# Optimization experiments

Measured on AMD Instinct MI355X. Metric: run time of the kernel, lower is better.

Reference implementation:

```python
import jax, jax.numpy as jnp
import numpy as np
from jax import lax

C = 512   # n_feat == Cn == Cdim (forced by DA_conv/CA_layer consistency)
H, W = 16, 32  # reshape_codebooks(512)
K = 3     # kernel_size
RED = 8   # reduction


def _lrelu(x):
    return jax.nn.leaky_relu(x, 0.1)


def _conv1x1(x, w, b=None):
    # x: (B,C,H,W), w: (O,C) -- torch Conv2d(.,.,1) weight squeezed
    y = jnp.einsum('oc,bchw->bohw', w, x)
    if b is not None:
        y = y + b[None, :, None, None]
    return y


def _conv3x3(x, w, b):
    # x: (B,C,H,W), w: (O,C,3,3) OIHW, padding=k//2 == SAME for odd k
    y = lax.conv_general_dilated(x, w, (1, 1), 'SAME',
                                 dimension_numbers=('NCHW', 'OIHW', 'NCHW'))
    return y + b[None, :, None, None]


def _da_conv(c, deg, kw1, kw2, pw, pb, caw1, caw2):
    # per-channel dynamic kernels from degradation vectors: (Cn, K*K)
    kern = (_lrelu(deg @ kw1.T) @ kw2.T).reshape(C, 1, K, K)
    # depthwise conv, groups = b1*c1 = C (b1 == 1)
    out = lax.conv_general_dilated(c, kern, (1, 1), 'SAME',
                                   feature_group_count=C,
                                   dimension_numbers=('NCHW', 'OIHW', 'NCHW'))
    out = _lrelu(out)
    out = _conv1x1(out, pw, pb)
    # CA_layer: deg reshaped to (1, Cn, 16, 32), channel attention, deg * att
    dr = deg.reshape(1, C, H, W)
    att = jax.nn.sigmoid(_conv1x1(_lrelu(_conv1x1(dr, caw1)), caw2))
    return out + dr * att


def setup_inputs() -> dict:
    key = jax.random.key(0)
    ks = jax.random.split(key, 16)
    n = lambda i, shape, s=0.05: jax.random.normal(ks[i], shape, dtype=jnp.float32) * s
    return dict(
        c=jax.random.normal(ks[0], (1, C, H, W), dtype=jnp.float32),
        deg=jax.random.normal(ks[1], (C, C), dtype=jnp.float32) * 0.1,
        k1_w1=n(2, (C, C)), k1_w2=n(3, (K * K, C)),
        p1_w=n(4, (C, C)), p1_b=jnp.zeros((C,), jnp.float32),
        ca1_w1=n(5, (C // RED, C)), ca1_w2=n(6, (C, C // RED)),
        conv1_w=n(7, (C, C, K, K)), conv1_b=jnp.zeros((C,), jnp.float32),
        k2_w1=n(8, (C, C)), k2_w2=n(9, (K * K, C)),
        p2_w=n(10, (C, C)), p2_b=jnp.zeros((C,), jnp.float32),
        ca2_w1=n(11, (C // RED, C)), ca2_w2=n(12, (C, C // RED)),
        conv2_w=n(13, (C, C, K, K)), conv2_b=jnp.zeros((C,), jnp.float32),
    )


def reference(c, deg, k1_w1, k1_w2, p1_w, p1_b, ca1_w1, ca1_w2,
              conv1_w, conv1_b, k2_w1, k2_w2, p2_w, p2_b,
              ca2_w1, ca2_w2, conv2_w, conv2_b):
    out = _lrelu(_da_conv(c, deg, k1_w1, k1_w2, p1_w, p1_b, ca1_w1, ca1_w2))
    out = _lrelu(_conv3x3(out, conv1_w, conv1_b))
    out = _lrelu(_da_conv(out, deg, k2_w1, k2_w2, p2_w, p2_b, ca2_w1, ca2_w2))
    return _conv3x3(out, conv2_w, conv2_b) + c
```

## Files before the change

kernel.cpp:

```cpp
#include <hip/hip_runtime.h>
#include <hip/hip_bf16.h>

typedef __attribute__((ext_vector_type(8))) unsigned short ushort8;
typedef __attribute__((ext_vector_type(8))) __bf16 bf16x8;
typedef __attribute__((ext_vector_type(4))) float f32x4;
typedef __attribute__((ext_vector_type(4))) unsigned short ushort4v;

__device__ __forceinline__ float lrelu_f(float v){ return v > 0.f ? v : 0.1f*v; }

__device__ __forceinline__ unsigned short f2bf(float v){
  unsigned u = __float_as_uint(v);
  unsigned r = (u + 0x7fffu + ((u>>16)&1u)) >> 16;
  return (unsigned short)r;
}
__device__ __forceinline__ float bf2f(unsigned short u){
  return __uint_as_float(((unsigned)u)<<16);
}

__device__ __forceinline__ void gload16(const void* g, void* l){
  __builtin_amdgcn_global_load_lds(
    (const __attribute__((address_space(1))) unsigned int*)g,
    (__attribute__((address_space(3))) unsigned int*)l, 16, 0, 0);
}

__device__ __forceinline__ void packq(const float* __restrict__ s,
                                      unsigned short* __restrict__ d, int i){
  const float4 v = ((const float4*)s)[i];
  ushort4v o; o.x=f2bf(v.x); o.y=f2bf(v.y); o.z=f2bf(v.z); o.w=f2bf(v.w);
  *(ushort4v*)(d + (size_t)i*4) = o;
}

__global__ __launch_bounds__(256) void k_pack_all(
  const float* __restrict__ k1_w1, const float* __restrict__ k2_w1,
  const float* __restrict__ p1_w,  const float* __restrict__ p2_w,
  const float* __restrict__ ca1_w1,const float* __restrict__ ca1_w2,
  const float* __restrict__ ca2_w1,const float* __restrict__ ca2_w2,
  const float* __restrict__ deg,   const float* __restrict__ conv1_w,
  const float* __restrict__ conv2_w,
  unsigned short* __restrict__ K1B, unsigned short* __restrict__ K2B,
  unsigned short* __restrict__ P1B, unsigned short* __restrict__ P2B,
  unsigned short* __restrict__ CA1A,unsigned short* __restrict__ CA1B,
  unsigned short* __restrict__ CA2A,unsigned short* __restrict__ CA2B,
  unsigned short* __restrict__ DEGB,unsigned short* __restrict__ DEGT,
  unsigned short* __restrict__ WB1, unsigned short* __restrict__ WB2){
  int i = blockIdx.x*256 + threadIdx.x;
  if (i < 65536){ packq(k1_w1, K1B, i); return; } i -= 65536;
  if (i < 65536){ packq(k2_w1, K2B, i); return; } i -= 65536;
  if (i < 65536){ packq(p1_w,  P1B, i); return; } i -= 65536;
  if (i < 65536){ packq(p2_w,  P2B, i); return; } i -= 65536;
  if (i < 8192){ packq(ca1_w1, CA1A, i); return; } i -= 8192;
  if (i < 8192){ packq(ca1_w2, CA1B, i); return; } i -= 8192;
  if (i < 8192){ packq(ca2_w1, CA2A, i); return; } i -= 8192;
  if (i < 8192){ packq(ca2_w2, CA2B, i); return; } i -= 8192;
  if (i < 65536){ packq(deg, DEGB, i); return; } i -= 65536;
  if (i < 65536){
    const int j = i*4; const int p = j>>9, c = j&511;
    ushort4v o;
    o.x = f2bf(deg[(size_t)(c+0)*512 + p]);
    o.y = f2bf(deg[(size_t)(c+1)*512 + p]);
    o.z = f2bf(deg[(size_t)(c+2)*512 + p]);
    o.w = f2bf(deg[(size_t)(c+3)*512 + p]);
    *(ushort4v*)(DEGT + (size_t)j) = o;
    return;
  } i -= 65536;
  if (i < 589824){
    const int o_ = i/1152; const int r4 = (i - o_*1152)*4;
    const int t = r4>>9; const int ci = r4&511;
    const float* s = conv1_w + (size_t)o_*4608;
    ushort4v o;
    o.x = f2bf(s[(ci+0)*9 + t]); o.y = f2bf(s[(ci+1)*9 + t]);
    o.z = f2bf(s[(ci+2)*9 + t]); o.w = f2bf(s[(ci+3)*9 + t]);
    *(ushort4v*)(WB1 + (size_t)o_*4608 + r4) = o;
    return;
  } i -= 589824;
  if (i < 589824){
    const int o_ = i/1152; const int r4 = (i - o_*1152)*4;
    const int t = r4>>9; const int ci = r4&511;
    const float* s = conv2_w + (size_t)o_*4608;
    ushort4v o;
    o.x = f2bf(s[(ci+0)*9 + t]); o.y = f2bf(s[(ci+1)*9 + t]);
    o.z = f2bf(s[(ci+2)*9 + t]); o.w = f2bf(s[(ci+3)*9 + t]);
    *(ushort4v*)(WB2 + (size_t)o_*4608 + r4) = o;
  }
}

__device__ __forceinline__ void gemm32(
    const unsigned short* __restrict__ A, const unsigned short* __restrict__ Bt,
    int m0, int n0, int K, int tid,
    unsigned short* lA, unsigned short* lB, f32x4& acc){
  const int wid = tid>>6, lane = tid&63;
  const int half = tid>>7, st_ = tid&127;
  const int srow = st_>>2, skb = st_&3;
  const unsigned short* gS = (half ? Bt + (size_t)(n0+srow)*K
                                   : A  + (size_t)(m0+srow)*K);
  unsigned short* lS = half ? lB : lA;
  const int soff0 = srow*64 + 8*(skb ^ (srow&7));
  const int soff1 = srow*64 + 8*((skb+4) ^ (srow&7));

  const int wr = (wid>>1)*16, wc = (wid&1)*16;
  const int l15 = lane&15, lkb = lane>>4;
  int aoff[2], boff[2];
  #pragma unroll
  for (int h=0;h<2;h++){
    const int Ra = wr + l15;
    aoff[h] = Ra*64 + 8*((lkb+4*h) ^ (Ra&7));
    const int Rb = wc + l15;
    boff[h] = Rb*64 + 8*((lkb+4*h) ^ (Rb&7));
  }

  const int nst = K>>6;
  ushort8 r0 = *(const ushort8*)(gS + skb*8);
  ushort8 r1 = *(const ushort8*)(gS + (skb+4)*8);
  *(ushort8*)(lS + soff0) = r0;
  *(ushort8*)(lS + soff1) = r1;
  if (nst > 1){
    r0 = *(const ushort8*)(gS + 64 + skb*8);
    r1 = *(const ushort8*)(gS + 64 + (skb+4)*8);
  }
  __syncthreads();
  for (int st=0; st<nst; ++st){
    const int cur = (st&1)*2048;
    bf16x8 af[2], bf[2];
    #pragma unroll
    for (int h=0;h<2;h++){
      af[h] = *(const bf16x8*)(lA + cur + aoff[h]);
      bf[h] = *(const bf16x8*)(lB + cur + boff[h]);
    }
    if (st+1 < nst){
      const int nxt = ((st+1)&1)*2048;
      *(ushort8*)(lS + nxt + soff0) = r0;
      *(ushort8*)(lS + nxt + soff1) = r1;
      if (st+2 < nst){
        r0 = *(const ushort8*)(gS + (size_t)(st+2)*64 + skb*8);
        r1 = *(const ushort8*)(gS + (size_t)(st+2)*64 + (skb+4)*8);
      }
    }
    #pragma unroll
    for (int h=0;h<2;h++)
      acc = __builtin_amdgcn_mfma_f32_16x16x32_bf16(af[h], bf[h], acc, 0,0,0);
    __syncthreads();
  }
}

__global__ __launch_bounds__(256) void k_mgemm_pre(
    const unsigned short* __restrict__ DEGB, const unsigned short* __restrict__ DEGT,
    const unsigned short* __restrict__ K1B,  const unsigned short* __restrict__ K2B,
    const unsigned short* __restrict__ CA1A, const unsigned short* __restrict__ CA2A,
    float* __restrict__ TMP1, float* __restrict__ TMP2,
    unsigned short* __restrict__ HID1, unsigned short* __restrict__ HID2){
  const int z = blockIdx.z;
  if (z >= 2 && blockIdx.y >= 2) return;
  const unsigned short* A  = (z < 2) ? DEGB : DEGT;
  const unsigned short* Bt = (z==0) ? K1B : (z==1) ? K2B : (z==2) ? CA1A : CA2A;
  __shared__ unsigned short lA[4096], lB[4096];
  const int tid = threadIdx.x;
  const int m0 = blockIdx.x*32, n0 = blockIdx.y*32;
  f32x4 acc = {};
  gemm32(A, Bt, m0, n0, 512, tid, lA, lB, acc);

  const int wid = tid>>6, lane = tid&63;
  const int wr = (wid>>1)*16, wc = (wid&1)*16;
  const int l15 = lane&15, lkb = lane>>4;
  #pragma unroll
  for (int r=0;r<4;r++){
    const int row = m0 + wr + lkb*4 + r;
    const int col = n0 + wc + l15;
    const float v = lrelu_f(acc[r]);
    if (z==0)      TMP1[(size_t)row*512 + col] = v;
    else if (z==1) TMP2[(size_t)row*512 + col] = v;
    else if (z==2) HID1[(size_t)row*64 + col] = f2bf(v);
    else           HID2[(size_t)row*64 + col] = f2bf(v);
  }
}

__device__ __forceinline__ void gemm64(
    const unsigned short* __restrict__ A, const unsigned short* __restrict__ Bt,
    int m0, int n0, int K, int tid,
    unsigned short* lA, unsigned short* lB, f32x4 acc[2][2]){
  const int wid = tid>>6, lane = tid&63;
  const int srow = tid>>2, skb = tid&3;
  const unsigned short* gA = A  + (size_t)(m0+srow)*K + skb*8;
  const unsigned short* gB = Bt + (size_t)(n0+srow)*K + skb*8;
  const int soff = srow*32 + 8*(skb ^ (srow&3));
  const int wr = (wid>>1)*32, wc = (wid&1)*32;
  const int l15 = lane&15, lkb = lane>>4;
  int aoff[2], boff[2];
  #pragma unroll
  for (int s=0;s<2;s++){
    const int Ra = wr + s*16 + l15;
    aoff[s] = Ra*32 + 8*(lkb ^ (Ra&3));
    const int Rb = wc + s*16 + l15;
    boff[s] = Rb*32 + 8*(lkb ^ (Rb&3));
  }
  const int nst = K>>5;
  ushort8 ra = *(const ushort8*)gA;
  ushort8 rb = *(const ushort8*)gB;
  *(ushort8*)(lA + soff) = ra;
  *(ushort8*)(lB + soff) = rb;
  if (nst > 1){ ra = *(const ushort8*)(gA+32); rb = *(const ushort8*)(gB+32); }
  __syncthreads();
  for (int st=0; st<nst; ++st){
    const int cur = (st&1)*2048;
    bf16x8 af[2], bfr[2];
    #pragma unroll
    for (int s=0;s<2;s++){
      af[s]  = *(const bf16x8*)(lA + cur + aoff[s]);
      bfr[s] = *(const bf16x8*)(lB + cur + boff[s]);
    }
    if (st+1 < nst){
      const int nxt = ((st+1)&1)*2048;
      *(ushort8*)(lA + nxt + soff) = ra;
      *(ushort8*)(lB + nxt + soff) = rb;
      if (st+2 < nst){
        ra = *(const ushort8*)(gA + (size_t)(st+2)*32);
        rb = *(const ushort8*)(gB + (size_t)(st+2)*32);
      }
    }
    #pragma unroll
    for (int mi=0;mi<2;mi++)
      #pragma unroll
      for (int ni=0;ni<2;ni++)
        acc[mi][ni] = __builtin_amdgcn_mfma_f32_16x16x32_bf16(af[mi], bfr[ni], acc[mi][ni], 0,0,0);
    __syncthreads();
  }
}

__global__ __launch_bounds__(256) void k_kern_att(
    const float* __restrict__ TMP1, const float* __restrict__ TMP2,
    const float* __restrict__ kw2a, const float* __restrict__ kw2b,
    const unsigned short* __restrict__ CA1B, const unsigned short* __restrict__ CA2B,
    const unsigned short* __restrict__ HID1, const unsigned short* __restrict__ HID2,
    float* __restrict__ kern0, float* __restrict__ kern1,
    float* __restrict__ ATT1, float* __restrict__ ATT2){
  const int z = blockIdx.z;
  const int tid = threadIdx.x;
  if (z < 2){
    const float* tmp  = z ? TMP2 : TMP1;
    const float* kw2  = z ? kw2b : kw2a;
    float* kern       = z ? kern1 : kern0;
    const int i = blockIdx.x*4 + (tid>>6);
    const int lane = tid&63;
    float acc[9];
    #pragma unroll
    for (int q=0;q<9;q++) acc[q]=0.f;
    for (int j=lane; j<512; j+=64){
      const float t = tmp[i*512 + j];
      #pragma unroll
      for (int q=0;q<9;q++) acc[q] += t*kw2[q*512 + j];
    }
    #pragma unroll
    for (int q=0;q<9;q++){
      float v = acc[q];
      #pragma unroll
      for (int off=32; off>0; off>>=1) v += __shfl_down(v, off);
      if (lane==0) kern[i*9+q] = v;
    }
  } else {
    if (blockIdx.x >= 64) return;
    const unsigned short* A  = (z==2) ? CA1B : CA2B;
    const unsigned short* Bt = (z==2) ? HID1 : HID2;
    float* ATT               = (z==2) ? ATT1 : ATT2;
    __shared__ unsigned short lA[4096], lB[4096];
    const int m0 = (blockIdx.x>>3)*64, n0 = (blockIdx.x&7)*64;
    f32x4 acc[2][2] = {};
    gemm64(A, Bt, m0, n0, 64, tid, lA, lB, acc);
    const int wid = tid>>6, lane = tid&63;
    const int wr = (wid>>1)*32, wc = (wid&1)*32;
    const int l15 = lane&15, lkb = lane>>4;
    #pragma unroll
    for (int mi=0;mi<2;mi++)
      #pragma unroll
      for (int ni=0;ni<2;ni++){
        const int row = m0 + wr + mi*16 + lkb*4;
        const int col = n0 + wc + ni*16 + l15;
        #pragma unroll
        for (int r=0;r<4;r++)
          ATT[(size_t)(row+r)*512 + col] = 1.f/(1.f + expf(-acc[mi][ni][r]));
      }
  }
}

__global__ __launch_bounds__(512) void k_dwconv(const float* __restrict__ x,
    const float* __restrict__ kern, unsigned short* __restrict__ yt,
    unsigned short* __restrict__ XTP){
  const int c = blockIdx.x;
  const int p = threadIdx.x;
  const int iy = p>>5, ix = p&31;
  {
    const int idx = blockIdx.x*512 + p;
    if (idx < 12800){
      const int si = idx>>7, wi = idx&127;
      int slot;
      if (si < 34) slot = si;
      else if (si < 68) slot = 578 + (si-34);
      else if (si < 84) slot = (si-67)*34;
      else slot = (si-83)*34 + 33;
      ushort4v z = {};
      *(ushort4v*)(XTP + (size_t)slot*512 + wi*4) = z;
    }
  }
  __shared__ float plane[18*34];
  for (int i=p;i<18*34;i+=512) plane[i]=0.f;
  __syncthreads();
  plane[(iy+1)*34 + ix+1] = x[c*512 + p];
  __syncthreads();
  const float* kp = kern + c*9;
  float s = 0.f;
  #pragma unroll
  for (int dy=0;dy<3;dy++)
    #pragma unroll
    for (int dx=0;dx<3;dx++)
      s += plane[(iy+dy)*34 + ix+dx]*kp[dy*3+dx];
  yt[(size_t)p*512 + c] = f2bf(lrelu_f(s));
}

__global__ __launch_bounds__(512) void k_dwconv_red(const unsigned short* __restrict__ part,
    const float* __restrict__ bias, const float* __restrict__ kern,
    unsigned short* __restrict__ yt, int nchunks){
  const int c = blockIdx.x;
  const int p = threadIdx.x;
  const int iy = p>>5, ix = p&31;
  __shared__ float plane[18*34];
  for (int i=p;i<18*34;i+=512) plane[i]=0.f;
  __syncthreads();
  if (p < 128){
    const float b = bias[c];
    float4 a4 = {b,b,b,b};
    for (int s=0;s<nchunks;s++){
      const ushort4v v = ((const ushort4v*)(part + (size_t)s*262144 + c*512))[p];
      a4.x += bf2f(v.x); a4.y += bf2f(v.y); a4.z += bf2f(v.z); a4.w += bf2f(v.w);
    }
    a4.x = lrelu_f(a4.x); a4.y = lrelu_f(a4.y);
    a4.z = lrelu_f(a4.z); a4.w = lrelu_f(a4.w);
    const int px0 = p*4;
    float* dst = &plane[((px0>>5)+1)*34 + (px0&31)+1];
    dst[0]=a4.x; dst[1]=a4.y; dst[2]=a4.z; dst[3]=a4.w;
  }
  __syncthreads();
  const float* kp = kern + c*9;
  float s = 0.f;
  #pragma unroll
  for (int dy=0;dy<3;dy++)
    #pragma unroll
    for (int dx=0;dx<3;dx++)
      s += plane[(iy+dy)*34 + ix+dx]*kp[dy*3+dx];
  yt[(size_t)p*512 + c] = f2bf(lrelu_f(s));
}

__global__ __launch_bounds__(256) void k_pw(
    const unsigned short* __restrict__ A, const unsigned short* __restrict__ Bt,
    const float* __restrict__ bias,
    const float* __restrict__ E1, const float* __restrict__ E2,
    unsigned short* __restrict__ XTP){
  __shared__ unsigned short lA[4096], lB[4096];
  __shared__ float tile[32][33];
  const int tid = threadIdx.x;
  const int wid = tid>>6, lane = tid&63;
  const int M0 = blockIdx.x*32, N0 = blockIdx.y*32;

  f32x4 acc = {};
  gemm32(A, Bt, M0, N0, 512, tid, lA, lB, acc);

  const int wr = (wid>>1)*16, wc = (wid&1)*16;
  const int l15 = lane&15, lkb = lane>>4;
  #pragma unroll
  for (int r=0;r<4;r++){
    const int rl = wr + lkb*4 + r;
    const int cl = wc + l15;
    const int rr = M0 + rl, col = N0 + cl;
    float v = acc[r] + bias[rr] + E1[(size_t)rr*512+col]*E2[(size_t)rr*512+col];
    tile[rl][cl] = lrelu_f(v);
  }
  __syncthreads();
  const int pr = tid>>3, q = tid&7;
  const int p = N0 + pr;
  const int slot = ((p>>5)+1)*34 + (p&31) + 1;
  ushort4v o;
  o.x = f2bf(tile[q*4+0][pr]); o.y = f2bf(tile[q*4+1][pr]);
  o.z = f2bf(tile[q*4+2][pr]); o.w = f2bf(tile[q*4+3][pr]);
  *(ushort4v*)(XTP + (size_t)slot*512 + M0 + q*4) = o;
}

template<int KCH>
__global__ __launch_bounds__(256) void k_mfma_conv(
    const unsigned short* __restrict__ WB,
    const unsigned short* __restrict__ XTP,
    unsigned short* __restrict__ part){
  __shared__ __attribute__((aligned(16))) unsigned short lA[2][4096];
  __shared__ __attribute__((aligned(16))) unsigned short lB[2][8192];
  const int tid = threadIdx.x;
  const int wid = tid>>6, lane = tid&63;
  const int m0 = blockIdx.x*64, n0 = blockIdx.y*128;
  const int k0 = blockIdx.z*KCH;

  const int wrow = wid*8 + (lane>>3);
  const int clin = lane&7;
  const unsigned short* asrc[2];
  #pragma unroll
  for (int j=0;j<2;j++){
    const int r = j*32 + wrow;
    asrc[j] = WB + (size_t)(m0+r)*4608 + k0 + (clin ^ (r&7))*8;
  }
  int bpy[4], bpx[4], bchk[4];
  #pragma unroll
  for (int j=0;j<4;j++){
    const int r = j*32 + wrow;
    const int pp = n0 + r;
    bpy[j] = pp>>5; bpx[j] = pp&31;
    bchk[j] = (clin ^ (r&7))*8;
  }

  const int wr = (wid>>1)*32, wc = (wid&1)*64;
  const int l15 = lane&15, lkb = lane>>4;
  int aoff[2][2], boff[4][2];
  #pragma unroll
  for (int s=0;s<2;s++){
    const int Ra = wr + s*16 + l15;
    #pragma unroll
    for (int h=0;h<2;h++) aoff[s][h] = Ra*64 + 8*((lkb+4*h) ^ (Ra&7));
  }
  #pragma unroll
  for (int u=0;u<4;u++){
    const int Rb = wc + u*16 + l15;
    #pragma unroll
    for (int h=0;h<2;h++) boff[u][h] = Rb*64 + 8*((lkb+4*h) ^ (Rb&7));
  }

  auto stage = [&](int buf, int st){
    #pragma unroll
    for (int j=0;j<2;j++)
      gload16(asrc[j] + st*64, &lA[buf][j*2048 + wid*512]);
    const int k = k0 + st*64;
    const int t = k>>9;
    const int dy = t/3, dx = t - dy*3;
    const int kc = k & 511;
    #pragma unroll
    for (int j=0;j<4;j++){
      const int slot = (bpy[j]+dy)*34 + bpx[j]+dx;
      gload16(XTP + (size_t)slot*512 + kc + bchk[j],
              &lB[buf][j*2048 + wid*512]);
    }
  };

  constexpr int NST = KCH/64;
  f32x4 acc[2][4] = {};
  stage(0, 0);
  __syncthreads();
  #pragma unroll
  for (int st=0; st<NST; ++st){
    const int cur = st&1;
    if (st+1 < NST) stage(cur^1, st+1);
    bf16x8 af[2][2], bfr[4][2];
    #pragma unroll
    for (int s=0;s<2;s++)
      #pragma unroll
      for (int h=0;h<2;h++) af[s][h] = *(const bf16x8*)(&lA[cur][aoff[s][h]]);
    #pragma unroll
    for (int u=0;u<4;u++)
      #pragma unroll
      for (int h=0;h<2;h++) bfr[u][h] = *(const bf16x8*)(&lB[cur][boff[u][h]]);
    #pragma unroll
    for (int h=0;h<2;h++)
      #pragma unroll
      for (int s=0;s<2;s++)
        #pragma unroll
        for (int u=0;u<4;u++)
          acc[s][u] = __builtin_amdgcn_mfma_f32_16x16x32_bf16(af[s][h], bfr[u][h], acc[s][u], 0,0,0);
    __syncthreads();
  }

  unsigned short* pbase = part + (size_t)blockIdx.z*262144;
  #pragma unroll
  for (int s=0;s<2;s++)
    #pragma unroll
    for (int u=0;u<4;u++){
      const int row = m0 + wr + s*16 + lkb*4;
      const int col = n0 + wc + u*16 + l15;
      #pragma unroll
      for (int r=0;r<4;r++)
        pbase[(size_t)(row+r)*512 + col] = f2bf(acc[s][u][r]);
    }
}

__global__ __launch_bounds__(256) void k_reduce_final(const unsigned short* __restrict__ part,
    const float* __restrict__ bias, const float* __restrict__ res,
    float* __restrict__ y, int nchunks){
  const int i = blockIdx.x*256 + threadIdx.x;
  const int o = i>>7;
  const float b = bias[o];
  float4 a4 = {b,b,b,b};
  for (int s=0;s<nchunks;s++){
    const ushort4v v = ((const ushort4v*)part)[(size_t)s*65536 + i];
    a4.x += bf2f(v.x); a4.y += bf2f(v.y); a4.z += bf2f(v.z); a4.w += bf2f(v.w);
  }
  const float4 rv = ((const float4*)res)[i];
  a4.x += rv.x; a4.y += rv.y; a4.z += rv.z; a4.w += rv.w;
  ((float4*)y)[i] = a4;
}

extern "C" void kernel_launch(void* const* d_in, const int* in_sizes, int n_in,
                              void* d_out, int out_size, void* d_ws, size_t ws_size,
                              hipStream_t stream) {
  (void)in_sizes; (void)n_in; (void)out_size; (void)ws_size;
  const float* xin    = (const float*)d_in[0];
  const float* deg    = (const float*)d_in[1];
  const float* k1_w1  = (const float*)d_in[2];
  const float* k1_w2  = (const float*)d_in[3];
  const float* p1_w   = (const float*)d_in[4];
  const float* p1_b   = (const float*)d_in[5];
  const float* ca1_w1 = (const float*)d_in[6];
  const float* ca1_w2 = (const float*)d_in[7];
  const float* conv1_w= (const float*)d_in[8];
  const float* conv1_b= (const float*)d_in[9];
  const float* k2_w1  = (const float*)d_in[10];
  const float* k2_w2  = (const float*)d_in[11];
  const float* p2_w   = (const float*)d_in[12];
  const float* p2_b   = (const float*)d_in[13];
  const float* ca2_w1 = (const float*)d_in[14];
  const float* ca2_w2 = (const float*)d_in[15];
  const float* conv2_w= (const float*)d_in[16];
  const float* conv2_b= (const float*)d_in[17];
  float* out = (float*)d_out;

  const int NS = 18;

  float* ws = (float*)d_ws;
  unsigned short* PART = (unsigned short*)ws;
  ws += (size_t)NS*131072;
  float* TMP1 = (float*)PART;
  float* TMP2 = TMP1 + 262144;
  unsigned short* HID1 = (unsigned short*)(TMP2 + 262144);
  unsigned short* HID2 = HID1 + 32768;
  float* KERN1 = ws;  ws += 4608;
  float* KERN2 = ws;  ws += 4608;
  float* ATT1  = ws;  ws += 262144;
  float* ATT2  = ws;  ws += 262144;
  unsigned short* DEGB = (unsigned short*)ws; ws += 131072;
  unsigned short* DEGT = (unsigned short*)ws; ws += 131072;
  unsigned short* K1B  = (unsigned short*)ws; ws += 131072;
  unsigned short* K2B  = (unsigned short*)ws; ws += 131072;
  unsigned short* XTP  = K1B;
  unsigned short* P1B  = (unsigned short*)ws; ws += 131072;
  unsigned short* P2B  = (unsigned short*)ws; ws += 131072;
  unsigned short* CA1A = (unsigned short*)ws; ws += 16384;
  unsigned short* CA1B = (unsigned short*)ws; ws += 16384;
  unsigned short* CA2A = (unsigned short*)ws; ws += 16384;
  unsigned short* CA2B = (unsigned short*)ws; ws += 16384;
  unsigned short* DWLT = (unsigned short*)ws; ws += 131072;
  unsigned short* WB1  = (unsigned short*)ws; ws += 1179648;
  unsigned short* WB2  = (unsigned short*)ws; ws += 1179648;

  k_pack_all<<<6272,256,0,stream>>>(k1_w1,k2_w1,p1_w,p2_w,
      ca1_w1,ca1_w2,ca2_w1,ca2_w2, deg, conv1_w, conv2_w,
      K1B,K2B,P1B,P2B, CA1A,CA1B,CA2A,CA2B, DEGB,DEGT, WB1,WB2);

  k_mgemm_pre<<<dim3(16,16,4),256,0,stream>>>(DEGB,DEGT, K1B,K2B, CA1A,CA2A,
      TMP1,TMP2, HID1,HID2);
  k_kern_att<<<dim3(128,1,4),256,0,stream>>>(TMP1,TMP2, k1_w2,k2_w2,
      CA1B,CA2B, HID1,HID2, KERN1,KERN2, ATT1,ATT2);

  k_dwconv<<<512,512,0,stream>>>(xin, KERN1, DWLT, XTP);
  k_pw<<<dim3(16,16),256,0,stream>>>(P1B, DWLT, p1_b, deg, ATT1, XTP);
  k_mfma_conv<256><<<dim3(8,4,18),256,0,stream>>>(WB1, XTP, PART);
  k_dwconv_red<<<512,512,0,stream>>>(PART, conv1_b, KERN2, DWLT, NS);
  k_pw<<<dim3(16,16),256,0,stream>>>(P2B, DWLT, p2_b, deg, ATT2, XTP);
  k_mfma_conv<256><<<dim3(8,4,18),256,0,stream>>>(WB2, XTP, PART);
  k_reduce_final<<<256,256,0,stream>>>(PART, conv2_b, xin, out, NS);
}
```

Measured before the change: 81.96 us.

## Fuse fp32-to-bf16 conversion into GEMM loads and merge pre-stage kernels

Drops the separate packing of most fp32 weights and deg to bf16. The GEMM tile loaders now convert fp32 to bf16 while loading from global memory. The dynamic-kernel second projection is fused into the first GEMM's epilogue as per-column-block partial sums, which the depthwise kernels reduce. The channel-attention GEMM and the first depthwise conv are merged into one launch, removing a kernel and the TMP round trips. The cost is that GEMMs now read fp32 from global memory, doubling load bytes and adding conversion work inside the K loop.

```diff
diff --git a/kernel.cpp b/kernel.cpp
--- a/kernel.cpp
+++ b/kernel.cpp
@@ -23,36 +23,24 @@
     (__attribute__((address_space(3))) unsigned int*)l, 16, 0, 0);
 }
 
-__device__ __forceinline__ void packq(const float* __restrict__ s,
-                                      unsigned short* __restrict__ d, int i){
-  const float4 v = ((const float4*)s)[i];
-  ushort4v o; o.x=f2bf(v.x); o.y=f2bf(v.y); o.z=f2bf(v.z); o.w=f2bf(v.w);
-  *(ushort4v*)(d + (size_t)i*4) = o;
-}
-
-__global__ __launch_bounds__(256) void k_pack_all(
-  const float* __restrict__ k1_w1, const float* __restrict__ k2_w1,
-  const float* __restrict__ p1_w,  const float* __restrict__ p2_w,
-  const float* __restrict__ ca1_w1,const float* __restrict__ ca1_w2,
-  const float* __restrict__ ca2_w1,const float* __restrict__ ca2_w2,
-  const float* __restrict__ deg,   const float* __restrict__ conv1_w,
+__device__ __forceinline__ ushort8 ld8(const unsigned short* p){
+  return *(const ushort8*)p;
+}
+__device__ __forceinline__ ushort8 ld8(const float* p){
+  const float4 a = *(const float4*)p;
+  const float4 b = *(const float4*)(p+4);
+  ushort8 o;
+  o[0]=f2bf(a.x); o[1]=f2bf(a.y); o[2]=f2bf(a.z); o[3]=f2bf(a.w);
+  o[4]=f2bf(b.x); o[5]=f2bf(b.y); o[6]=f2bf(b.z); o[7]=f2bf(b.w);
+  return o;
+}
+
+__global__ __launch_bounds__(256) void k_pack_lite(
+  const float* __restrict__ deg, const float* __restrict__ conv1_w,
   const float* __restrict__ conv2_w,
-  unsigned short* __restrict__ K1B, unsigned short* __restrict__ K2B,
-  unsigned short* __restrict__ P1B, unsigned short* __restrict__ P2B,
-  unsigned short* __restrict__ CA1A,unsigned short* __restrict__ CA1B,
-  unsigned short* __restrict__ CA2A,unsigned short* __restrict__ CA2B,
-  unsigned short* __restrict__ DEGB,unsigned short* __restrict__ DEGT,
+  unsigned short* __restrict__ DEGT,
   unsigned short* __restrict__ WB1, unsigned short* __restrict__ WB2){
   int i = blockIdx.x*256 + threadIdx.x;
-  if (i < 65536){ packq(k1_w1, K1B, i); return; } i -= 65536;
-  if (i < 65536){ packq(k2_w1, K2B, i); return; } i -= 65536;
-  if (i < 65536){ packq(p1_w,  P1B, i); return; } i -= 65536;
-  if (i < 65536){ packq(p2_w,  P2B, i); return; } i -= 65536;
-  if (i < 8192){ packq(ca1_w1, CA1A, i); return; } i -= 8192;
-  if (i < 8192){ packq(ca1_w2, CA1B, i); return; } i -= 8192;
-  if (i < 8192){ packq(ca2_w1, CA2A, i); return; } i -= 8192;
-  if (i < 8192){ packq(ca2_w2, CA2B, i); return; } i -= 8192;
-  if (i < 65536){ packq(deg, DEGB, i); return; } i -= 65536;
   if (i < 65536){
     const int j = i*4; const int p = j>>9, c = j&511;
     ushort4v o;
@@ -63,36 +51,28 @@
     *(ushort4v*)(DEGT + (size_t)j) = o;
     return;
   } i -= 65536;
-  if (i < 589824){
-    const int o_ = i/1152; const int r4 = (i - o_*1152)*4;
-    const int t = r4>>9; const int ci = r4&511;
-    const float* s = conv1_w + (size_t)o_*4608;
-    ushort4v o;
-    o.x = f2bf(s[(ci+0)*9 + t]); o.y = f2bf(s[(ci+1)*9 + t]);
-    o.z = f2bf(s[(ci+2)*9 + t]); o.w = f2bf(s[(ci+3)*9 + t]);
-    *(ushort4v*)(WB1 + (size_t)o_*4608 + r4) = o;
-    return;
-  } i -= 589824;
-  if (i < 589824){
-    const int o_ = i/1152; const int r4 = (i - o_*1152)*4;
-    const int t = r4>>9; const int ci = r4&511;
-    const float* s = conv2_w + (size_t)o_*4608;
-    ushort4v o;
-    o.x = f2bf(s[(ci+0)*9 + t]); o.y = f2bf(s[(ci+1)*9 + t]);
-    o.z = f2bf(s[(ci+2)*9 + t]); o.w = f2bf(s[(ci+3)*9 + t]);
-    *(ushort4v*)(WB2 + (size_t)o_*4608 + r4) = o;
-  }
-}
-
+  const float* src; unsigned short* dst;
+  if (i < 589824){ src = conv1_w; dst = WB1; }
+  else { i -= 589824; if (i >= 589824) return; src = conv2_w; dst = WB2; }
+  const int o_ = i/1152; const int r4 = (i - o_*1152)*4;
+  const int t = r4>>9; const int ci = r4&511;
+  const float* s = src + (size_t)o_*4608;
+  ushort4v o;
+  o.x = f2bf(s[(ci+0)*9 + t]); o.y = f2bf(s[(ci+1)*9 + t]);
+  o.z = f2bf(s[(ci+2)*9 + t]); o.w = f2bf(s[(ci+3)*9 + t]);
+  *(ushort4v*)(dst + (size_t)o_*4608 + r4) = o;
+}
+
+template<typename TA, typename TB>
 __device__ __forceinline__ void gemm32(
-    const unsigned short* __restrict__ A, const unsigned short* __restrict__ Bt,
+    const TA* __restrict__ A, const TB* __restrict__ Bt,
     int m0, int n0, int K, int tid,
     unsigned short* lA, unsigned short* lB, f32x4& acc){
   const int wid = tid>>6, lane = tid&63;
   const int half = tid>>7, st_ = tid&127;
   const int srow = st_>>2, skb = st_&3;
-  const unsigned short* gS = (half ? Bt + (size_t)(n0+srow)*K
-                                   : A  + (size_t)(m0+srow)*K);
+  const TA* gSa = A  + (size_t)(m0+srow)*K;
+  const TB* gSb = Bt + (size_t)(n0+srow)*K;
   unsigned short* lS = half ? lB : lA;
   const int soff0 = srow*64 + 8*(skb ^ (srow&7));
   const int soff1 = srow*64 + 8*((skb+4) ^ (srow&7));
@@ -109,13 +89,14 @@
   }
 
   const int nst = K>>6;
-  ushort8 r0 = *(const ushort8*)(gS + skb*8);
-  ushort8 r1 = *(const ushort8*)(gS + (skb+4)*8);
+  ushort8 r0, r1;
+  if (half==0){ r0 = ld8(gSa + skb*8); r1 = ld8(gSa + (skb+4)*8); }
+  else        { r0 = ld8(gSb + skb*8); r1 = ld8(gSb + (skb+4)*8); }
   *(ushort8*)(lS + soff0) = r0;
   *(ushort8*)(lS + soff1) = r1;
   if (nst > 1){
-    r0 = *(const ushort8*)(gS + 64 + skb*8);
-    r1 = *(const ushort8*)(gS + 64 + (skb+4)*8);
+    if (half==0){ r0 = ld8(gSa + 64 + skb*8); r1 = ld8(gSa + 64 + (skb+4)*8); }
+    else        { r0 = ld8(gSb + 64 + skb*8); r1 = ld8(gSb + 64 + (skb+4)*8); }
   }
   __syncthreads();
   for (int st=0; st<nst; ++st){
@@ -131,8 +112,10 @@
       *(ushort8*)(lS + nxt + soff0) = r0;
       *(ushort8*)(lS + nxt + soff1) = r1;
       if (st+2 < nst){
-        r0 = *(const ushort8*)(gS + (size_t)(st+2)*64 + skb*8);
-        r1 = *(const ushort8*)(gS + (size_t)(st+2)*64 + (skb+4)*8);
+        if (half==0){ r0 = ld8(gSa + (size_t)(st+2)*64 + skb*8);
+                      r1 = ld8(gSa + (size_t)(st+2)*64 + (skb+4)*8); }
+        else        { r0 = ld8(gSb + (size_t)(st+2)*64 + skb*8);
+                      r1 = ld8(gSb + (size_t)(st+2)*64 + (skb+4)*8); }
       }
     }
     #pragma unroll
@@ -142,45 +125,15 @@
   }
 }
 
-__global__ __launch_bounds__(256) void k_mgemm_pre(
-    const unsigned short* __restrict__ DEGB, const unsigned short* __restrict__ DEGT,
-    const unsigned short* __restrict__ K1B,  const unsigned short* __restrict__ K2B,
-    const unsigned short* __restrict__ CA1A, const unsigned short* __restrict__ CA2A,
-    float* __restrict__ TMP1, float* __restrict__ TMP2,
-    unsigned short* __restrict__ HID1, unsigned short* __restrict__ HID2){
-  const int z = blockIdx.z;
-  if (z >= 2 && blockIdx.y >= 2) return;
-  const unsigned short* A  = (z < 2) ? DEGB : DEGT;
-  const unsigned short* Bt = (z==0) ? K1B : (z==1) ? K2B : (z==2) ? CA1A : CA2A;
-  __shared__ unsigned short lA[4096], lB[4096];
-  const int tid = threadIdx.x;
-  const int m0 = blockIdx.x*32, n0 = blockIdx.y*32;
-  f32x4 acc = {};
-  gemm32(A, Bt, m0, n0, 512, tid, lA, lB, acc);
-
-  const int wid = tid>>6, lane = tid&63;
-  const int wr = (wid>>1)*16, wc = (wid&1)*16;
-  const int l15 = lane&15, lkb = lane>>4;
-  #pragma unroll
-  for (int r=0;r<4;r++){
-    const int row = m0 + wr + lkb*4 + r;
-    const int col = n0 + wc + l15;
-    const float v = lrelu_f(acc[r]);
-    if (z==0)      TMP1[(size_t)row*512 + col] = v;
-    else if (z==1) TMP2[(size_t)row*512 + col] = v;
-    else if (z==2) HID1[(size_t)row*64 + col] = f2bf(v);
-    else           HID2[(size_t)row*64 + col] = f2bf(v);
-  }
-}
-
+template<typename TA, typename TB>
 __device__ __forceinline__ void gemm64(
-    const unsigned short* __restrict__ A, const unsigned short* __restrict__ Bt,
+    const TA* __restrict__ A, const TB* __restrict__ Bt,
     int m0, int n0, int K, int tid,
     unsigned short* lA, unsigned short* lB, f32x4 acc[2][2]){
   const int wid = tid>>6, lane = tid&63;
   const int srow = tid>>2, skb = tid&3;
-  const unsigned short* gA = A  + (size_t)(m0+srow)*K + skb*8;
-  const unsigned short* gB = Bt + (size_t)(n0+srow)*K + skb*8;
+  const TA* gA = A  + (size_t)(m0+srow)*K + skb*8;
+  const TB* gB = Bt + (size_t)(n0+srow)*K + skb*8;
   const int soff = srow*32 + 8*(skb ^ (srow&3));
   const int wr = (wid>>1)*32, wc = (wid&1)*32;
   const int l15 = lane&15, lkb = lane>>4;
@@ -193,11 +146,11 @@
     boff[s] = Rb*32 + 8*(lkb ^ (Rb&3));
   }
   const int nst = K>>5;
-  ushort8 ra = *(const ushort8*)gA;
-  ushort8 rb = *(const ushort8*)gB;
+  ushort8 ra = ld8(gA);
+  ushort8 rb = ld8(gB);
   *(ushort8*)(lA + soff) = ra;
   *(ushort8*)(lB + soff) = rb;
-  if (nst > 1){ ra = *(const ushort8*)(gA+32); rb = *(const ushort8*)(gB+32); }
+  if (nst > 1){ ra = ld8(gA+32); rb = ld8(gB+32); }
   __syncthreads();
   for (int st=0; st<nst; ++st){
     const int cur = (st&1)*2048;
@@ -212,8 +165,8 @@
       *(ushort8*)(lA + nxt + soff) = ra;
       *(ushort8*)(lB + nxt + soff) = rb;
       if (st+2 < nst){
-        ra = *(const ushort8*)(gA + (size_t)(st+2)*32);
-        rb = *(const ushort8*)(gB + (size_t)(st+2)*32);
+        ra = ld8(gA + (size_t)(st+2)*32);
+        rb = ld8(gB + (size_t)(st+2)*32);
       }
     }
     #pragma unroll
@@ -225,45 +178,87 @@
   }
 }
 
-__global__ __launch_bounds__(256) void k_kern_att(
-    const float* __restrict__ TMP1, const float* __restrict__ TMP2,
+__global__ __launch_bounds__(256) void k_pre(
+    const float* __restrict__ deg, const unsigned short* __restrict__ DEGT,
+    const float* __restrict__ k1_w1, const float* __restrict__ k2_w1,
+    const float* __restrict__ ca1_w1, const float* __restrict__ ca2_w1,
     const float* __restrict__ kw2a, const float* __restrict__ kw2b,
-    const unsigned short* __restrict__ CA1B, const unsigned short* __restrict__ CA2B,
-    const unsigned short* __restrict__ HID1, const unsigned short* __restrict__ HID2,
-    float* __restrict__ kern0, float* __restrict__ kern1,
-    float* __restrict__ ATT1, float* __restrict__ ATT2){
+    float* __restrict__ KP1, float* __restrict__ KP2,
+    unsigned short* __restrict__ HID1, unsigned short* __restrict__ HID2){
+  __shared__ unsigned short lA[4096], lB[4096];
+  __shared__ float kp[2][32][9];
   const int z = blockIdx.z;
   const int tid = threadIdx.x;
+  const int wid = tid>>6, lane = tid&63;
+  const int l15 = lane&15, lkb = lane>>4;
+
   if (z < 2){
-    const float* tmp  = z ? TMP2 : TMP1;
-    const float* kw2  = z ? kw2b : kw2a;
-    float* kern       = z ? kern1 : kern0;
-    const int i = blockIdx.x*4 + (tid>>6);
-    const int lane = tid&63;
-    float acc[9];
-    #pragma unroll
-    for (int q=0;q<9;q++) acc[q]=0.f;
-    for (int j=lane; j<512; j+=64){
-      const float t = tmp[i*512 + j];
-      #pragma unroll
-      for (int q=0;q<9;q++) acc[q] += t*kw2[q*512 + j];
-    }
-    #pragma unroll
-    for (int q=0;q<9;q++){
-      float v = acc[q];
-      #pragma unroll
-      for (int off=32; off>0; off>>=1) v += __shfl_down(v, off);
-      if (lane==0) kern[i*9+q] = v;
+    const int it = blockIdx.x, jc = blockIdx.y;
+    const float* kw1 = z ? k2_w1 : k1_w1;
+    const float* kw2 = z ? kw2b : kw2a;
+    float* KP        = z ? KP2 : KP1;
+    const int m0 = it*32, n0 = jc*32;
+    f32x4 acc = {};
+    gemm32(deg, kw1, m0, n0, 512, tid, lA, lB, acc);
+
+    const int wr = (wid>>1)*16, wc2 = wid&1;
+    const int col = jc*32 + wc2*16 + l15;
+    float w[9];
+    #pragma unroll
+    for (int t=0;t<9;t++) w[t] = kw2[t*512 + col];
+    #pragma unroll
+    for (int r=0;r<4;r++){
+      const float v = lrelu_f(acc[r]);
+      const int row = wr + lkb*4 + r;
+      #pragma unroll
+      for (int t=0;t<9;t++){
+        float q = v*w[t];
+        q += __shfl_xor(q,1); q += __shfl_xor(q,2);
+        q += __shfl_xor(q,4); q += __shfl_xor(q,8);
+        if (l15==0) kp[wc2][row][t] = q;
+      }
+    }
+    __syncthreads();
+    for (int i = tid; i < 288; i += 256){
+      const int row = i/9, t = i - row*9;
+      KP[((size_t)jc*512 + m0 + row)*9 + t] = kp[0][row][t] + kp[1][row][t];
     }
   } else {
-    if (blockIdx.x >= 64) return;
-    const unsigned short* A  = (z==2) ? CA1B : CA2B;
-    const unsigned short* Bt = (z==2) ? HID1 : HID2;
-    float* ATT               = (z==2) ? ATT1 : ATT2;
-    __shared__ unsigned short lA[4096], lB[4096];
-    const int m0 = (blockIdx.x>>3)*64, n0 = (blockIdx.x&7)*64;
+    if (blockIdx.y >= 2) return;
+    const float* caw = (z==2) ? ca1_w1 : ca2_w1;
+    unsigned short* HID = (z==2) ? HID1 : HID2;
+    const int m0 = blockIdx.x*32, n0 = blockIdx.y*32;
+    f32x4 acc = {};
+    gemm32(DEGT, caw, m0, n0, 512, tid, lA, lB, acc);
+    const int wr = (wid>>1)*16, wc = (wid&1)*16;
+    #pragma unroll
+    for (int r=0;r<4;r++){
+      const int row = m0 + wr + lkb*4 + r;
+      const int col = n0 + wc + l15;
+      HID[(size_t)row*64 + col] = f2bf(lrelu_f(acc[r]));
+    }
+  }
+}
+
+__global__ __launch_bounds__(256) void k_att_dw(
+    const float* __restrict__ ca1_w2, const float* __restrict__ ca2_w2,
+    const unsigned short* __restrict__ HID1, const unsigned short* __restrict__ HID2,
+    float* __restrict__ ATT1, float* __restrict__ ATT2,
+    const float* __restrict__ xin, const float* __restrict__ KP1,
+    unsigned short* __restrict__ DWLT, unsigned short* __restrict__ XTP){
+  __shared__ __align__(16) unsigned char smem[16640];
+  const int tid = threadIdx.x;
+  int bid = blockIdx.x;
+  if (bid < 128){
+    unsigned short* lA = (unsigned short*)smem;
+    unsigned short* lB = lA + 4096;
+    const int b = bid>>6, t6 = bid&63;
+    const float* caw          = b ? ca2_w2 : ca1_w2;
+    const unsigned short* HID = b ? HID2 : HID1;
+    float* ATT                = b ? ATT2 : ATT1;
+    const int m0 = (t6>>3)*64, n0 = (t6&7)*64;
     f32x4 acc[2][2] = {};
-    gemm64(A, Bt, m0, n0, 64, tid, lA, lB, acc);
+    gemm64(caw, HID, m0, n0, 64, tid, lA, lB, acc);
     const int wid = tid>>6, lane = tid&63;
     const int wr = (wid>>1)*32, wc = (wid&1)*32;
     const int l15 = lane&15, lkb = lane>>4;
@@ -277,51 +272,67 @@
         for (int r=0;r<4;r++)
           ATT[(size_t)(row+r)*512 + col] = 1.f/(1.f + expf(-acc[mi][ni][r]));
       }
-  }
-}
-
-__global__ __launch_bounds__(512) void k_dwconv(const float* __restrict__ x,
-    const float* __restrict__ kern, unsigned short* __restrict__ yt,
-    unsigned short* __restrict__ XTP){
-  const int c = blockIdx.x;
-  const int p = threadIdx.x;
-  const int iy = p>>5, ix = p&31;
-  {
-    const int idx = blockIdx.x*512 + p;
-    if (idx < 12800){
-      const int si = idx>>7, wi = idx&127;
-      int slot;
-      if (si < 34) slot = si;
-      else if (si < 68) slot = 578 + (si-34);
-      else if (si < 84) slot = (si-67)*34;
-      else slot = (si-83)*34 + 33;
-      ushort4v z = {};
-      *(ushort4v*)(XTP + (size_t)slot*512 + wi*4) = z;
-    }
-  }
-  __shared__ float plane[18*34];
-  for (int i=p;i<18*34;i+=512) plane[i]=0.f;
-  __syncthreads();
-  plane[(iy+1)*34 + ix+1] = x[c*512 + p];
-  __syncthreads();
-  const float* kp = kern + c*9;
-  float s = 0.f;
-  #pragma unroll
-  for (int dy=0;dy<3;dy++)
-    #pragma unroll
-    for (int dx=0;dx<3;dx++)
-      s += plane[(iy+dy)*34 + ix+dx]*kp[dy*3+dx];
-  yt[(size_t)p*512 + c] = f2bf(lrelu_f(s));
+  } else {
+    bid -= 128;
+    const int c = bid;
+    {
+      const int idx = bid*256 + tid;
+      if (idx < 12800){
+        const int si = idx>>7, wi = idx&127;
+        int slot;
+        if (si < 34) slot = si;
+        else if (si < 68) slot = 578 + (si-34);
+        else if (si < 84) slot = (si-67)*34;
+        else slot = (si-83)*34 + 33;
+        ushort4v zz = {};
+        *(ushort4v*)(XTP + (size_t)slot*512 + wi*4) = zz;
+      }
+    }
+    float* plane = (float*)smem;
+    float* ks = plane + 612;
+    for (int i=tid;i<612;i+=256) plane[i]=0.f;
+    if (tid<9){
+      float s=0.f;
+      #pragma unroll
+      for (int jc=0;jc<16;jc++) s += KP1[((size_t)jc*512 + c)*9 + tid];
+      ks[tid]=s;
+    }
+    #pragma unroll
+    for (int q=0;q<2;q++){
+      const int px = tid + q*256;
+      plane[((px>>5)+1)*34 + (px&31)+1] = xin[(size_t)c*512 + px];
+    }
+    __syncthreads();
+    #pragma unroll
+    for (int q=0;q<2;q++){
+      const int px = tid + q*256;
+      const int iy = px>>5, ix = px&31;
+      float s = 0.f;
+      #pragma unroll
+      for (int dy=0;dy<3;dy++)
+        #pragma unroll
+        for (int dx=0;dx<3;dx++)
+          s += plane[(iy+dy)*34 + ix+dx]*ks[dy*3+dx];
+      DWLT[(size_t)px*512 + c] = f2bf(lrelu_f(s));
+    }
+  }
 }
 
 __global__ __launch_bounds__(512) void k_dwconv_red(const unsigned short* __restrict__ part,
-    const float* __restrict__ bias, const float* __restrict__ kern,
+    const float* __restrict__ bias, const float* __restrict__ KP,
     unsigned short* __restrict__ yt, int nchunks){
   const int c = blockIdx.x;
   const int p = threadIdx.x;
   const int iy = p>>5, ix = p&31;
   __shared__ float plane[18*34];
+  __shared__ float ks[9];
   for (int i=p;i<18*34;i+=512) plane[i]=0.f;
+  if (p < 9){
+    float s = 0.f;
+    #pragma unroll
+    for (int jc=0;jc<16;jc++) s += KP[((size_t)jc*512 + c)*9 + p];
+    ks[p] = s;
+  }
   __syncthreads();
   if (p < 128){
     const float b = bias[c];
@@ -337,18 +348,17 @@
     dst[0]=a4.x; dst[1]=a4.y; dst[2]=a4.z; dst[3]=a4.w;
   }
   __syncthreads();
-  const float* kp = kern + c*9;
   float s = 0.f;
   #pragma unroll
   for (int dy=0;dy<3;dy++)
     #pragma unroll
     for (int dx=0;dx<3;dx++)
-      s += plane[(iy+dy)*34 + ix+dx]*kp[dy*3+dx];
+      s += plane[(iy+dy)*34 + ix+dx]*ks[dy*3+dx];
   yt[(size_t)p*512 + c] = f2bf(lrelu_f(s));
 }
 
 __global__ __launch_bounds__(256) void k_pw(
-    const unsigned short* __restrict__ A, const unsigned short* __restrict__ Bt,
+    const float* __restrict__ A, const unsigned short* __restrict__ Bt,
     const float* __restrict__ bias,
     const float* __restrict__ E1, const float* __restrict__ E2,
     unsigned short* __restrict__ XTP){
@@ -525,45 +535,31 @@
   const int NS = 18;
 
   float* ws = (float*)d_ws;
-  unsigned short* PART = (unsigned short*)ws;
-  ws += (size_t)NS*131072;
-  float* TMP1 = (float*)PART;
-  float* TMP2 = TMP1 + 262144;
-  unsigned short* HID1 = (unsigned short*)(TMP2 + 262144);
-  unsigned short* HID2 = HID1 + 32768;
-  float* KERN1 = ws;  ws += 4608;
-  float* KERN2 = ws;  ws += 4608;
-  float* ATT1  = ws;  ws += 262144;
-  float* ATT2  = ws;  ws += 262144;
-  unsigned short* DEGB = (unsigned short*)ws; ws += 131072;
+  unsigned short* PART = (unsigned short*)ws;  ws += (size_t)NS*131072;
+  float* KP1  = ws;  ws += 73728;
+  float* KP2  = ws;  ws += 73728;
+  float* ATT1 = ws;  ws += 262144;
+  float* ATT2 = ws;  ws += 262144;
+  unsigned short* HID1 = (unsigned short*)ws; ws += 16384;
+  unsigned short* HID2 = (unsigned short*)ws; ws += 16384;
   unsigned short* DEGT = (unsigned short*)ws; ws += 131072;
-  unsigned short* K1B  = (unsigned short*)ws; ws += 131072;
-  unsigned short* K2B  = (unsigned short*)ws; ws += 131072;
-  unsigned short* XTP  = K1B;
-  unsigned short* P1B  = (unsigned short*)ws; ws += 131072;
-  unsigned short* P2B  = (unsigned short*)ws; ws += 131072;
-  unsigned short* CA1A = (unsigned short*)ws; ws += 16384;
-  unsigned short* CA1B = (unsigned short*)ws; ws += 16384;
-  unsigned short* CA2A = (unsigned short*)ws; ws += 16384;
-  unsigned short* CA2B = (unsigned short*)ws; ws += 16384;
+  unsigned short* XTP  = (unsigned short*)ws; ws += 156672;
   unsigned short* DWLT = (unsigned short*)ws; ws += 131072;
   unsigned short* WB1  = (unsigned short*)ws; ws += 1179648;
   unsigned short* WB2  = (unsigned short*)ws; ws += 1179648;
 
-  k_pack_all<<<6272,256,0,stream>>>(k1_w1,k2_w1,p1_w,p2_w,
-      ca1_w1,ca1_w2,ca2_w1,ca2_w2, deg, conv1_w, conv2_w,
-      K1B,K2B,P1B,P2B, CA1A,CA1B,CA2A,CA2B, DEGB,DEGT, WB1,WB2);
-
-  k_mgemm_pre<<<dim3(16,16,4),256,0,stream>>>(DEGB,DEGT, K1B,K2B, CA1A,CA2A,
-      TMP1,TMP2, HID1,HID2);
-  k_kern_att<<<dim3(128,1,4),256,0,stream>>>(TMP1,TMP2, k1_w2,k2_w2,
-      CA1B,CA2B, HID1,HID2, KERN1,KERN2, ATT1,ATT2);
-
-  k_dwconv<<<512,512,0,stream>>>(xin, KERN1, DWLT, XTP);
-  k_pw<<<dim3(16,16),256,0,stream>>>(P1B, DWLT, p1_b, deg, ATT1, XTP);
+  k_pack_lite<<<4864,256,0,stream>>>(deg, conv1_w, conv2_w, DEGT, WB1, WB2);
+
+  k_pre<<<dim3(16,16,4),256,0,stream>>>(deg, DEGT, k1_w1, k2_w1,
+      ca1_w1, ca2_w1, k1_w2, k2_w2, KP1, KP2, HID1, HID2);
+
+  k_att_dw<<<640,256,0,stream>>>(ca1_w2, ca2_w2, HID1, HID2, ATT1, ATT2,
+      xin, KP1, DWLT, XTP);
+
+  k_pw<<<dim3(16,16),256,0,stream>>>(p1_w, DWLT, p1_b, deg, ATT1, XTP);
   k_mfma_conv<256><<<dim3(8,4,18),256,0,stream>>>(WB1, XTP, PART);
-  k_dwconv_red<<<512,512,0,stream>>>(PART, conv1_b, KERN2, DWLT, NS);
-  k_pw<<<dim3(16,16),256,0,stream>>>(P2B, DWLT, p2_b, deg, ATT2, XTP);
+  k_dwconv_red<<<512,512,0,stream>>>(PART, conv1_b, KP2, DWLT, NS);
+  k_pw<<<dim3(16,16),256,0,stream>>>(p2_w, DWLT, p2_b, deg, ATT2, XTP);
   k_mfma_conv<256><<<dim3(8,4,18),256,0,stream>>>(WB2, XTP, PART);
   k_reduce_final<<<256,256,0,stream>>>(PART, conv2_b, xin, out, NS);
 }
```

Result: slower. 86.45 us (+5.5%).
